# Performance work log

Measured on AMD Instinct MI355X. Metric: run time of the kernel, lower is better.

The kernel has to match this reference:

```python
import jax, jax.numpy as jnp
import numpy as np

BS, S, H = 16, 2048, 1024
D = 32           # num_discourse spans per example
C = 8            # num_discourse_types + 1 classifiers
L = 3            # num_labels


def setup_inputs() -> dict:
    key = jax.random.key(0)
    k1, k2, k3, k4, k5 = jax.random.split(key, 5)
    encoder_layer = jax.random.normal(k1, (BS, S, H), dtype=jnp.float32)
    W = jax.random.normal(k2, (C, H, L), dtype=jnp.float32) * 0.02
    b = jnp.zeros((C, L), dtype=jnp.float32)
    # non-overlapping spans partitioning the sequence: head = d*chunk, tail = head+chunk
    chunk = S // D  # 64; pooled slice is [head+1 : tail], length 63 (matches a+1:b)
    head = jnp.tile(jnp.arange(D, dtype=jnp.int64)[None, :] * chunk, (BS, 1))
    tail = head + chunk
    discourse_type_ids = jax.random.randint(k3, (BS, D), 0, C)
    labels = jax.random.randint(k4, (BS, D), 0, L)
    return {
        "encoder_layer": encoder_layer,
        "W": W,
        "b": b,
        "span_head_idxs": head,
        "span_tail_idxs": tail,
        "discourse_type_ids": discourse_type_ids,
        "labels": labels,
    }


def _forward(encoder_layer, W, b, span_head_idxs, span_tail_idxs,
             discourse_type_ids, labels):
    # ragged per-span mean pooling over encoder_layer[i, a+1:b]
    pos = jnp.arange(S)                                   # [S]
    mask = ((pos[None, None, :] >= span_head_idxs[:, :, None] + 1)
            & (pos[None, None, :] < span_tail_idxs[:, :, None]))  # [B,D,S]
    maskf = mask.astype(encoder_layer.dtype)
    counts = jnp.sum(maskf, axis=-1, keepdims=True)        # [B,D,1]
    pooled = jnp.einsum('bds,bsh->bdh', maskf, encoder_layer) / counts  # [B,D,H]
    # (dropout is identity in eval)
    # all 8 classifiers, then gather per discourse type
    all_logits = jnp.einsum('bdh,chl->bdcl', pooled, W) + b[None, None]  # [B,D,C,L]
    idx = discourse_type_ids[:, :, None, None]            # [B,D,1,1]
    logits = jnp.take_along_axis(all_logits, idx, axis=2).squeeze(2)    # [B,D,L]
    # cross entropy with ignore_index=-1
    valid = (labels >= 0)
    safe = jnp.where(valid, labels, 0)
    logp = jax.nn.log_softmax(logits, axis=-1)            # [B,D,L]
    nll = -jnp.take_along_axis(logp, safe[..., None], axis=-1).squeeze(-1)
    validf = valid.astype(logits.dtype)
    loss = jnp.sum(nll * validf) / jnp.sum(validf)
    return logits, loss


def reference(encoder_layer, W, b, span_head_idxs, span_tail_idxs,
              discourse_type_ids, labels):
    return _forward(encoder_layer, W, b, span_head_idxs, span_tail_idxs,
                    discourse_type_ids, labels)
```

## Files before the change

kernel.cpp:

```cpp
#include <hip/hip_runtime.h>
#include <math.h>

#define BS 16
#define SS 2048
#define HH 1024
#define DD 32
#define CC 8
#define LL 3

__global__ __launch_bounds__(1024) void pool_logits_kernel(
    const float* __restrict__ enc,
    const float* __restrict__ W,
    const float* __restrict__ bias,
    const int*   __restrict__ head,
    const int*   __restrict__ tail,
    const int*   __restrict__ dt,
    float* __restrict__ logits)
{
    const int bd = blockIdx.x;
    const int b  = bd / DD;
    const int s0 = head[bd] + 1;
    const int s1 = tail[bd];
    const int c  = dt[bd];
    const int tid = threadIdx.x;
    const int cg  = tid & 255;
    const int rg  = tid >> 8;
    const int col = cg * 4;

    const float* base = enc + ((size_t)b * SS) * HH + col;

    float4 a0 = make_float4(0.f, 0.f, 0.f, 0.f);
    float4 a1 = a0;

    int s = s0 + rg;
    for (; s + 4 < s1; s += 8) {
        float4 v0 = *(const float4*)(base + (size_t)(s    ) * HH);
        float4 v1 = *(const float4*)(base + (size_t)(s + 4) * HH);
        a0.x += v0.x; a0.y += v0.y; a0.z += v0.z; a0.w += v0.w;
        a1.x += v1.x; a1.y += v1.y; a1.z += v1.z; a1.w += v1.w;
    }
    if (s < s1) {
        float4 v0 = *(const float4*)(base + (size_t)s * HH);
        a0.x += v0.x; a0.y += v0.y; a0.z += v0.z; a0.w += v0.w;
    }
    a0.x += a1.x; a0.y += a1.y; a0.z += a1.z; a0.w += a1.w;

    __shared__ float4 red[1024];
    red[tid] = a0;
    __syncthreads();

    if (tid < 256) {
        float4 p0 = red[tid];
        float4 p1 = red[tid + 256];
        float4 p2 = red[tid + 512];
        float4 p3 = red[tid + 768];
        float px = p0.x + p1.x + p2.x + p3.x;
        float py = p0.y + p1.y + p2.y + p3.y;
        float pz = p0.z + p1.z + p2.z + p3.z;
        float pw = p0.w + p1.w + p2.w + p3.w;

        const int cnt = s1 - s0;
        const float inv = (cnt > 0) ? (1.0f / (float)cnt) : 0.0f;
        px *= inv; py *= inv; pz *= inv; pw *= inv;

        const float* wp = W + ((size_t)c * HH + col) * LL;
        float l0 = px * wp[0] + py * wp[3] + pz * wp[6] + pw * wp[9];
        float l1 = px * wp[1] + py * wp[4] + pz * wp[7] + pw * wp[10];
        float l2 = px * wp[2] + py * wp[5] + pz * wp[8] + pw * wp[11];

        #pragma unroll
        for (int off = 32; off >= 1; off >>= 1) {
            l0 += __shfl_down(l0, off, 64);
            l1 += __shfl_down(l1, off, 64);
            l2 += __shfl_down(l2, off, 64);
        }
        __shared__ float ws[4][3];
        const int lane = tid & 63, wv = tid >> 6;
        if (lane == 0) { ws[wv][0] = l0; ws[wv][1] = l1; ws[wv][2] = l2; }
        __syncthreads();
        if (tid == 0) {
            float r0 = 0.f, r1 = 0.f, r2 = 0.f;
            #pragma unroll
            for (int w = 0; w < 4; ++w) { r0 += ws[w][0]; r1 += ws[w][1]; r2 += ws[w][2]; }
            logits[bd * LL + 0] = r0 + bias[c * LL + 0];
            logits[bd * LL + 1] = r1 + bias[c * LL + 1];
            logits[bd * LL + 2] = r2 + bias[c * LL + 2];
        }
    }
}

__global__ __launch_bounds__(512) void loss_kernel(
    const float* __restrict__ logits,
    const int*   __restrict__ labels,
    float* __restrict__ out_loss)
{
    const int i = threadIdx.x;
    float nll = 0.f, v = 0.f;
    {
        const int lab = labels[i];
        const float x0 = logits[i * LL + 0];
        const float x1 = logits[i * LL + 1];
        const float x2 = logits[i * LL + 2];
        const float m  = fmaxf(x0, fmaxf(x1, x2));
        const float lse = m + logf(expf(x0 - m) + expf(x1 - m) + expf(x2 - m));
        if (lab >= 0) {
            const float xl = (lab == 0) ? x0 : ((lab == 1) ? x1 : x2);
            nll = lse - xl;
            v   = 1.f;
        }
    }
    #pragma unroll
    for (int off = 32; off >= 1; off >>= 1) {
        nll += __shfl_down(nll, off, 64);
        v   += __shfl_down(v,   off, 64);
    }
    __shared__ float sn[8], sv[8];
    const int lane = i & 63, wv = i >> 6;
    if (lane == 0) { sn[wv] = nll; sv[wv] = v; }
    __syncthreads();
    if (i == 0) {
        float tn = 0.f, tv = 0.f;
        #pragma unroll
        for (int w = 0; w < 8; ++w) { tn += sn[w]; tv += sv[w]; }
        out_loss[0] = (tv > 0.f) ? (tn / tv) : 0.f;
    }
}

extern "C" void kernel_launch(void* const* d_in, const int* in_sizes, int n_in,
                              void* d_out, int out_size, void* d_ws, size_t ws_size,
                              hipStream_t stream) {
    const float* enc   = (const float*)d_in[0];
    const float* W     = (const float*)d_in[1];
    const float* bias  = (const float*)d_in[2];
    const int*   head  = (const int*)d_in[3];
    const int*   tail  = (const int*)d_in[4];
    const int*   dt    = (const int*)d_in[5];
    const int*   labels= (const int*)d_in[6];
    float* out = (float*)d_out;

    pool_logits_kernel<<<BS * DD, 1024, 0, stream>>>(enc, W, bias, head, tail, dt, out);
    loss_kernel<<<1, 512, 0, stream>>>(out, labels, out + BS * DD * LL);
}
```

Baseline: 203.4 us.

## Split each span across four 256-thread blocks and reduce partial logits in loss kernel

The pooling kernel now runs four 256-thread blocks per span instead of one 1024-thread block. Each block sums every fourth row and projects its partial mean straight onto the classifier weights, writing three partial logits to workspace. The loss kernel adds the four partials plus bias to produce the logits before computing the cross entropy. This removes the 16KB shared-memory float4 reduction and a block-wide barrier, gives 2048 smaller blocks for better occupancy and scheduling, and unrolls the row loop deeper for more loads in flight. In exchange it needs workspace memory, and each span's W slice is now read four times.

```diff
diff --git a/kernel.cpp b/kernel.cpp
--- a/kernel.cpp
+++ b/kernel.cpp
@@ -8,100 +8,99 @@
 #define CC 8
 #define LL 3
 
-__global__ __launch_bounds__(1024) void pool_logits_kernel(
+__global__ __launch_bounds__(256, 8) void pool_partial_kernel(
     const float* __restrict__ enc,
     const float* __restrict__ W,
-    const float* __restrict__ bias,
     const int*   __restrict__ head,
     const int*   __restrict__ tail,
     const int*   __restrict__ dt,
-    float* __restrict__ logits)
+    float* __restrict__ partials)
 {
-    const int bd = blockIdx.x;
-    const int b  = bd / DD;
-    const int s0 = head[bd] + 1;
-    const int s1 = tail[bd];
-    const int c  = dt[bd];
-    const int tid = threadIdx.x;
-    const int cg  = tid & 255;
-    const int rg  = tid >> 8;
-    const int col = cg * 4;
+    const int blk  = blockIdx.x;
+    const int bd   = blk >> 2;
+    const int part = blk & 3;
+    const int b    = bd >> 5;
+    const int s0   = head[bd] + 1;
+    const int s1   = tail[bd];
+    const int c    = dt[bd];
+    const int tid  = threadIdx.x;
+    const int col  = tid << 2;
 
     const float* base = enc + ((size_t)b * SS) * HH + col;
 
     float4 a0 = make_float4(0.f, 0.f, 0.f, 0.f);
     float4 a1 = a0;
 
-    int s = s0 + rg;
-    for (; s + 4 < s1; s += 8) {
-        float4 v0 = *(const float4*)(base + (size_t)(s    ) * HH);
-        float4 v1 = *(const float4*)(base + (size_t)(s + 4) * HH);
+    int s = s0 + part;
+    for (; s + 12 < s1; s += 16) {
+        float4 v0 = *(const float4*)(base + (size_t)(s     ) * HH);
+        float4 v1 = *(const float4*)(base + (size_t)(s +  4) * HH);
+        float4 v2 = *(const float4*)(base + (size_t)(s +  8) * HH);
+        float4 v3 = *(const float4*)(base + (size_t)(s + 12) * HH);
         a0.x += v0.x; a0.y += v0.y; a0.z += v0.z; a0.w += v0.w;
         a1.x += v1.x; a1.y += v1.y; a1.z += v1.z; a1.w += v1.w;
+        a0.x += v2.x; a0.y += v2.y; a0.z += v2.z; a0.w += v2.w;
+        a1.x += v3.x; a1.y += v3.y; a1.z += v3.z; a1.w += v3.w;
     }
-    if (s < s1) {
-        float4 v0 = *(const float4*)(base + (size_t)s * HH);
-        a0.x += v0.x; a0.y += v0.y; a0.z += v0.z; a0.w += v0.w;
+    for (; s < s1; s += 4) {
+        float4 v = *(const float4*)(base + (size_t)s * HH);
+        a0.x += v.x; a0.y += v.y; a0.z += v.z; a0.w += v.w;
     }
-    a0.x += a1.x; a0.y += a1.y; a0.z += a1.z; a0.w += a1.w;
 
-    __shared__ float4 red[1024];
-    red[tid] = a0;
+    const int   cnt = s1 - s0;
+    const float inv = (cnt > 0) ? (1.0f / (float)cnt) : 0.0f;
+    const float px = (a0.x + a1.x) * inv;
+    const float py = (a0.y + a1.y) * inv;
+    const float pz = (a0.z + a1.z) * inv;
+    const float pw = (a0.w + a1.w) * inv;
+
+    const float* wp = W + ((size_t)c * HH + col) * LL;
+    float l0 = px * wp[0] + py * wp[3] + pz * wp[6] + pw * wp[9];
+    float l1 = px * wp[1] + py * wp[4] + pz * wp[7] + pw * wp[10];
+    float l2 = px * wp[2] + py * wp[5] + pz * wp[8] + pw * wp[11];
+
+    #pragma unroll
+    for (int off = 32; off >= 1; off >>= 1) {
+        l0 += __shfl_down(l0, off, 64);
+        l1 += __shfl_down(l1, off, 64);
+        l2 += __shfl_down(l2, off, 64);
+    }
+    __shared__ float ws[4][3];
+    const int lane = tid & 63, wv = tid >> 6;
+    if (lane == 0) { ws[wv][0] = l0; ws[wv][1] = l1; ws[wv][2] = l2; }
     __syncthreads();
-
-    if (tid < 256) {
-        float4 p0 = red[tid];
-        float4 p1 = red[tid + 256];
-        float4 p2 = red[tid + 512];
-        float4 p3 = red[tid + 768];
-        float px = p0.x + p1.x + p2.x + p3.x;
-        float py = p0.y + p1.y + p2.y + p3.y;
-        float pz = p0.z + p1.z + p2.z + p3.z;
-        float pw = p0.w + p1.w + p2.w + p3.w;
-
-        const int cnt = s1 - s0;
-        const float inv = (cnt > 0) ? (1.0f / (float)cnt) : 0.0f;
-        px *= inv; py *= inv; pz *= inv; pw *= inv;
-
-        const float* wp = W + ((size_t)c * HH + col) * LL;
-        float l0 = px * wp[0] + py * wp[3] + pz * wp[6] + pw * wp[9];
-        float l1 = px * wp[1] + py * wp[4] + pz * wp[7] + pw * wp[10];
-        float l2 = px * wp[2] + py * wp[5] + pz * wp[8] + pw * wp[11];
-
-        #pragma unroll
-        for (int off = 32; off >= 1; off >>= 1) {
-            l0 += __shfl_down(l0, off, 64);
-            l1 += __shfl_down(l1, off, 64);
-            l2 += __shfl_down(l2, off, 64);
-        }
-        __shared__ float ws[4][3];
-        const int lane = tid & 63, wv = tid >> 6;
-        if (lane == 0) { ws[wv][0] = l0; ws[wv][1] = l1; ws[wv][2] = l2; }
-        __syncthreads();
-        if (tid == 0) {
-            float r0 = 0.f, r1 = 0.f, r2 = 0.f;
-            #pragma unroll
-            for (int w = 0; w < 4; ++w) { r0 += ws[w][0]; r1 += ws[w][1]; r2 += ws[w][2]; }
-            logits[bd * LL + 0] = r0 + bias[c * LL + 0];
-            logits[bd * LL + 1] = r1 + bias[c * LL + 1];
-            logits[bd * LL + 2] = r2 + bias[c * LL + 2];
-        }
+    if (tid == 0) {
+        float r0 = ws[0][0] + ws[1][0] + ws[2][0] + ws[3][0];
+        float r1 = ws[0][1] + ws[1][1] + ws[2][1] + ws[3][1];
+        float r2 = ws[0][2] + ws[1][2] + ws[2][2] + ws[3][2];
+        partials[blk * 3 + 0] = r0;
+        partials[blk * 3 + 1] = r1;
+        partials[blk * 3 + 2] = r2;
     }
 }
 
 __global__ __launch_bounds__(512) void loss_kernel(
-    const float* __restrict__ logits,
+    const float* __restrict__ partials,
+    const float* __restrict__ bias,
+    const int*   __restrict__ dt,
     const int*   __restrict__ labels,
-    float* __restrict__ out_loss)
+    float* __restrict__ out)
 {
     const int i = threadIdx.x;
+    const int c = dt[i];
+    const float4* p = (const float4*)(partials + (size_t)i * 12);
+    const float4 q0 = p[0], q1 = p[1], q2 = p[2];
+    const float x0 = q0.x + q0.w + q1.z + q2.y + bias[c * LL + 0];
+    const float x1 = q0.y + q1.x + q1.w + q2.z + bias[c * LL + 1];
+    const float x2 = q0.z + q1.y + q2.x + q2.w + bias[c * LL + 2];
+    out[i * LL + 0] = x0;
+    out[i * LL + 1] = x1;
+    out[i * LL + 2] = x2;
+
     float nll = 0.f, v = 0.f;
     {
         const int lab = labels[i];
-        const float x0 = logits[i * LL + 0];
-        const float x1 = logits[i * LL + 1];
-        const float x2 = logits[i * LL + 2];
-        const float m  = fmaxf(x0, fmaxf(x1, x2));
+        const float m   = fmaxf(x0, fmaxf(x1, x2));
         const float lse = m + logf(expf(x0 - m) + expf(x1 - m) + expf(x2 - m));
         if (lab >= 0) {
             const float xl = (lab == 0) ? x0 : ((lab == 1) ? x1 : x2);
@@ -122,22 +121,23 @@
         float tn = 0.f, tv = 0.f;
         #pragma unroll
         for (int w = 0; w < 8; ++w) { tn += sn[w]; tv += sv[w]; }
-        out_loss[0] = (tv > 0.f) ? (tn / tv) : 0.f;
+        out[BS * DD * LL] = (tv > 0.f) ? (tn / tv) : 0.f;
     }
 }
 
 extern "C" void kernel_launch(void* const* d_in, const int* in_sizes, int n_in,
                               void* d_out, int out_size, void* d_ws, size_t ws_size,
                               hipStream_t stream) {
-    const float* enc   = (const float*)d_in[0];
-    const float* W     = (const float*)d_in[1];
-    const float* bias  = (const float*)d_in[2];
-    const int*   head  = (const int*)d_in[3];
-    const int*   tail  = (const int*)d_in[4];
-    const int*   dt    = (const int*)d_in[5];
-    const int*   labels= (const int*)d_in[6];
-    float* out = (float*)d_out;
+    const float* enc    = (const float*)d_in[0];
+    const float* W      = (const float*)d_in[1];
+    const float* bias   = (const float*)d_in[2];
+    const int*   head   = (const int*)d_in[3];
+    const int*   tail   = (const int*)d_in[4];
+    const int*   dt     = (const int*)d_in[5];
+    const int*   labels = (const int*)d_in[6];
+    float* out      = (float*)d_out;
+    float* partials = (float*)d_ws;
 
-    pool_logits_kernel<<<BS * DD, 1024, 0, stream>>>(enc, W, bias, head, tail, dt, out);
-    loss_kernel<<<1, 512, 0, stream>>>(out, labels, out + BS * DD * LL);
+    pool_partial_kernel<<<BS * DD * 4, 256, 0, stream>>>(enc, W, head, tail, dt, partials);
+    loss_kernel<<<1, 512, 0, stream>>>(partials, bias, dt, labels, out);
 }
```

Result: no change. 202.1 us (-0.7%).
